# Optimization experiments

Hardware: AMD Instinct MI355X
Metric: run time of the kernel (lower is better)

## Reference

```python
import jax, jax.numpy as jnp
import numpy as np

N = 50000          # nodes
E = 600000         # edges
D = 128            # g_dim = h1_dim = h2_dim
R = 8              # 2 * n_speakers**2, n_speakers=2
B = 10             # num_bases


def setup_inputs() -> dict:
    key = jax.random.key(0)
    ks = jax.random.split(key, 10)
    s = 1.0 / np.sqrt(D)
    return {
        "node_features": jax.random.normal(ks[0], (N, D), jnp.float32),
        "edge_index": jax.random.randint(ks[1], (2, E), 0, N, jnp.int64),
        "edge_type": jax.random.randint(ks[2], (E,), 0, R, jnp.int64),
        # RGCNConv params (basis decomposition)
        "basis": jax.random.normal(ks[3], (B, D, D), jnp.float32) * s,
        "comp": jax.random.normal(ks[4], (R, B), jnp.float32) * (1.0 / np.sqrt(B)),
        "root": jax.random.normal(ks[5], (D, D), jnp.float32) * s,
        "bias1": jnp.zeros((D,), jnp.float32),
        # GraphConv params
        "w_rel": jax.random.normal(ks[6], (D, D), jnp.float32) * s,
        "b_rel": jnp.zeros((D,), jnp.float32),
        "w_root": jax.random.normal(ks[7], (D, D), jnp.float32) * s,
    }


def reference(node_features, edge_index, edge_type, basis, comp, root, bias1, w_rel, b_rel, w_root):
    x = node_features
    n = x.shape[0]
    r = comp.shape[0]
    src, dst = edge_index[0], edge_index[1]

    # ---- RGCNConv (basis decomposition, per-relation mean aggregation) ----
    # project through bases once: [N, B, D]
    xb = jnp.einsum('ni,bio->nbo', x, basis)
    # per-edge message: combine bases with relation coefficients  [E, D]
    msg = jnp.einsum('eb,ebo->eo', comp[edge_type], xb[src])
    # per-(dst, relation) mean normalization
    seg = dst * r + edge_type                       # [E]
    cnt = jax.ops.segment_sum(jnp.ones((msg.shape[0],), x.dtype), seg, num_segments=n * r)
    norm = 1.0 / jnp.maximum(cnt[seg], 1.0)         # [E]
    agg = jax.ops.segment_sum(msg * norm[:, None], dst, num_segments=n)  # [N, D]
    h1 = agg + x @ root + bias1

    # ---- GraphConv (add aggregation of neighbors + root transform) ----
    nbr = jax.ops.segment_sum(h1[src], dst, num_segments=n)  # [N, D]
    out = nbr @ w_rel.T + b_rel + h1 @ w_root.T
    return out
```

## Files before the change

### kernel.cpp

```cpp
#include <hip/hip_runtime.h>
#include <stdint.h>

#define N_NODES 50000
#define E_EDGES 600000
#define D 128
#define R_REL 8
#define B_BASES 10
#define RN (R_REL * N_NODES)

typedef __attribute__((ext_vector_type(8))) short bf16x8;
typedef __attribute__((ext_vector_type(4))) float f32x4;

__device__ __forceinline__ short f2b(float f) {
    uint32_t u = __float_as_uint(f);
    u += 0x7fff + ((u >> 16) & 1);
    return (short)(u >> 16);
}
__device__ __forceinline__ float b2f(uint16_t u) {
    return __uint_as_float((uint32_t)u << 16);
}

__global__ __launch_bounds__(256) void k_front(const float* __restrict__ x,
                                               unsigned short* __restrict__ xb,
                                               const int* __restrict__ dst,
                                               const int* __restrict__ et,
                                               int* __restrict__ cntr,
                                               const float* __restrict__ basis,
                                               const float* __restrict__ comp,
                                               const float* __restrict__ root,
                                               const float* __restrict__ wrel,
                                               const float* __restrict__ wroot,
                                               short* __restrict__ wt,
                                               short* __restrict__ wrel_b,
                                               short* __restrict__ wroot_b) {
    const int XB_N = N_NODES * D / 8;
    int tid = blockIdx.x * 256 + threadIdx.x;
    if (tid < XB_N) {
        const float4* s = (const float4*)x + (size_t)tid * 2;
        float4 v0 = s[0], v1 = s[1];
        union { uint4 u; unsigned short h[8]; } pk;
        pk.h[0] = (unsigned short)f2b(v0.x); pk.h[1] = (unsigned short)f2b(v0.y);
        pk.h[2] = (unsigned short)f2b(v0.z); pk.h[3] = (unsigned short)f2b(v0.w);
        pk.h[4] = (unsigned short)f2b(v1.x); pk.h[5] = (unsigned short)f2b(v1.y);
        pk.h[6] = (unsigned short)f2b(v1.z); pk.h[7] = (unsigned short)f2b(v1.w);
        ((uint4*)xb)[tid] = pk.u;
    } else if (tid < XB_N + E_EDGES) {
        int e = tid - XB_N;
        atomicAdd(&cntr[dst[e] * R_REL + et[e]], 1);
    } else {
        int t2 = tid - XB_N - E_EDGES;
        if (t2 < 9 * D * D) {
            int s = t2 >> 14;
            int rem = t2 & 16383;
            int j = rem >> 7, i = rem & 127;
            float v;
            if (s < 8) {
                v = 0.f;
#pragma unroll
                for (int b = 0; b < B_BASES; b++)
                    v += comp[s * B_BASES + b] * basis[b * D * D + i * D + j];
            } else {
                v = root[i * D + j];
            }
            wt[t2] = f2b(v);
        } else {
            int t3 = t2 - 9 * D * D;
            if (t3 < D * D) {
                wrel_b[t3]  = f2b(wrel[t3]);
                wroot_b[t3] = f2b(wroot[t3]);
            }
        }
    }
}

__device__ __forceinline__ int wave_scan_incl(int v) {
    int lane = threadIdx.x & 63;
#pragma unroll
    for (int off = 1; off < 64; off <<= 1) {
        int n = __shfl_up(v, off, 64);
        if (lane >= off) v += n;
    }
    return v;
}

__global__ __launch_bounds__(1024) void k_scan_a(const int* __restrict__ in,
                                                 int* __restrict__ out,
                                                 int* __restrict__ bsum, int n) {
    __shared__ int wsum[16];
    int t = threadIdx.x, lane = t & 63, wid = t >> 6;
    int g = blockIdx.x * 1024 + t;
    int v = (g < n) ? in[g] : 0;
    int isc = wave_scan_incl(v);
    if (lane == 63) wsum[wid] = isc;
    __syncthreads();
    if (wid == 0) {
        int wv = (lane < 16) ? wsum[lane] : 0;
        int wsc = wave_scan_incl(wv);
        if (lane < 16) wsum[lane] = wsc - wv;
    }
    __syncthreads();
    if (g < n) out[g] = wsum[wid] + isc - v;
    if (t == 1023 && bsum) bsum[blockIdx.x] = wsum[15] + isc;
}

__global__ __launch_bounds__(1024) void k_scan_c(int* __restrict__ out,
                                                 const int* __restrict__ bsum, int n) {
    int g = blockIdx.x * 1024 + threadIdx.x;
    if (g < n) out[g] += bsum[blockIdx.x];
}

__global__ __launch_bounds__(256) void k_bucket(const int* __restrict__ src,
                                                const int* __restrict__ dst,
                                                const int* __restrict__ et,
                                                int* __restrict__ seg_off,
                                                int* __restrict__ es1) {
    int e = blockIdx.x * 256 + threadIdx.x;
    if (e >= E_EDGES) return;
    int key = dst[e] * R_REL + et[e];
    int pos = atomicAdd(&seg_off[key], 1);
    es1[pos] = src[e];
}

__global__ __launch_bounds__(256) void k_aggmean(const unsigned short* __restrict__ xb,
                                                 const int* __restrict__ es1,
                                                 const int* __restrict__ seg_off,
                                                 unsigned short* __restrict__ mx) {
    int t = threadIdx.x;
    int sw = t >> 4, l = t & 15;
    int k = blockIdx.x * 16 + sw;
    if (k >= RN) return;
    int start = (k == 0) ? 0 : seg_off[k - 1];
    int end = seg_off[k];
    float ax[8];
#pragma unroll
    for (int q = 0; q < 8; q++) ax[q] = 0.f;
    size_t loff = (size_t)l * 8;
    int pos = start;
    for (; pos + 2 <= end; pos += 2) {
        int s0 = es1[pos], s1 = es1[pos + 1];
        uint4 v0 = *(const uint4*)(xb + (size_t)s0 * D + loff);
        uint4 v1 = *(const uint4*)(xb + (size_t)s1 * D + loff);
        const uint32_t* w0 = (const uint32_t*)&v0;
        const uint32_t* w1 = (const uint32_t*)&v1;
#pragma unroll
        for (int q = 0; q < 4; q++) {
            ax[q * 2]     += b2f((uint16_t)w0[q]) + b2f((uint16_t)w1[q]);
            ax[q * 2 + 1] += b2f((uint16_t)(w0[q] >> 16)) + b2f((uint16_t)(w1[q] >> 16));
        }
    }
    if (pos < end) {
        int s0 = es1[pos];
        uint4 v0 = *(const uint4*)(xb + (size_t)s0 * D + loff);
        const uint32_t* w0 = (const uint32_t*)&v0;
#pragma unroll
        for (int q = 0; q < 4; q++) {
            ax[q * 2]     += b2f((uint16_t)w0[q]);
            ax[q * 2 + 1] += b2f((uint16_t)(w0[q] >> 16));
        }
    }
    float nm = (end > start) ? 1.f / (float)(end - start) : 0.f;
    union { uint4 u; unsigned short h[8]; } pk;
#pragma unroll
    for (int q = 0; q < 8; q++) pk.h[q] = (unsigned short)f2b(ax[q] * nm);
    *(uint4*)(mx + (size_t)k * D + loff) = pk.u;
}

__global__ __launch_bounds__(256) void k_h1_gemm(const unsigned short* __restrict__ mx,
                                                 const unsigned short* __restrict__ xb,
                                                 const short* __restrict__ wt,
                                                 const float* __restrict__ bias1,
                                                 unsigned short* __restrict__ h1b) {
    __shared__ short ws[2][128 * 128];
    int t = threadIdx.x;
    int wave = t >> 6, lane = t & 63, quad = lane >> 4, l16 = lane & 15;
    int base = blockIdx.x * 128;
    int n0 = base + wave * 32 + l16;
    int n1 = n0 + 16;
    int nc0 = n0 < N_NODES ? n0 : N_NODES - 1;
    int nc1 = n1 < N_NODES ? n1 : N_NODES - 1;
    int ci0 = wave * 8;

    auto aptr = [&](int nc, int s) -> const unsigned short* {
        return (s < 8) ? mx + ((size_t)nc * 8 + s) * D : xb + (size_t)nc * D;
    };

    uint4 aReg[2][2][4];
    {
        uint4 b0[8];
#pragma unroll
        for (int i = 0; i < 8; i++) {
            int row = (ci0 + i) * 4 + quad;
            b0[i] = *(const uint4*)(wt + row * D + (l16 << 3));
        }
#pragma unroll
        for (int kc = 0; kc < 4; kc++) {
            int co = (kc * 4 + quad) * 8;
            aReg[0][0][kc] = *(const uint4*)(aptr(nc0, 0) + co);
            aReg[0][1][kc] = *(const uint4*)(aptr(nc1, 0) + co);
            aReg[1][0][kc] = *(const uint4*)(aptr(nc0, 1) + co);
            aReg[1][1][kc] = *(const uint4*)(aptr(nc1, 1) + co);
        }
#pragma unroll
        for (int i = 0; i < 8; i++) {
            int row = (ci0 + i) * 4 + quad;
            *(uint4*)&ws[0][row * 128 + ((l16 ^ (row & 15)) << 3)] = b0[i];
        }
    }
    __syncthreads();

    f32x4 acc[2][8];
#pragma unroll
    for (int tl = 0; tl < 2; tl++)
#pragma unroll
        for (int jt = 0; jt < 8; jt++) acc[tl][jt] = (f32x4){0.f, 0.f, 0.f, 0.f};

    for (int s = 0; s < 9; s++) {
        int cur = s & 1;
        uint4 bn[8];
        if (s + 1 < 9) {
            const short* wb = wt + (size_t)(s + 1) * D * D;
#pragma unroll
            for (int i = 0; i < 8; i++) {
                int row = (ci0 + i) * 4 + quad;
                bn[i] = *(const uint4*)(wb + row * D + (l16 << 3));
            }
        }
#pragma unroll
        for (int kc = 0; kc < 4; kc++) {
            int c0 = kc * 4 + quad;
            bf16x8 a0 = *(bf16x8*)&aReg[cur][0][kc];
            bf16x8 a1 = *(bf16x8*)&aReg[cur][1][kc];
#pragma unroll
            for (int jt = 0; jt < 8; jt++) {
                bf16x8 b = *(const bf16x8*)&ws[cur][(jt * 16 + l16) * 128 + ((c0 ^ l16) << 3)];
                acc[0][jt] = __builtin_amdgcn_mfma_f32_16x16x32_bf16(a0, b, acc[0][jt], 0, 0, 0);
                acc[1][jt] = __builtin_amdgcn_mfma_f32_16x16x32_bf16(a1, b, acc[1][jt], 0, 0, 0);
            }
        }
        if (s + 2 <= 8) {
#pragma unroll
            for (int kc = 0; kc < 4; kc++) {
                int co = (kc * 4 + quad) * 8;
                aReg[cur][0][kc] = *(const uint4*)(aptr(nc0, s + 2) + co);
                aReg[cur][1][kc] = *(const uint4*)(aptr(nc1, s + 2) + co);
            }
        }
        if (s + 1 < 9) {
#pragma unroll
            for (int i = 0; i < 8; i++) {
                int row = (ci0 + i) * 4 + quad;
                *(uint4*)&ws[cur ^ 1][row * 128 + ((l16 ^ (row & 15)) << 3)] = bn[i];
            }
        }
        __syncthreads();
    }

#pragma unroll
    for (int tl = 0; tl < 2; tl++) {
#pragma unroll
        for (int reg = 0; reg < 4; reg++) {
            int node = base + wave * 32 + tl * 16 + quad * 4 + reg;
            if (node >= N_NODES) continue;
#pragma unroll
            for (int jt = 0; jt < 8; jt++) {
                int col = jt * 16 + l16;
                float v = acc[tl][jt][reg] + bias1[col];
                h1b[(size_t)node * D + col] = (unsigned short)f2b(v);
            }
        }
    }
}

__global__ __launch_bounds__(256) void k_agg_nbr(const unsigned short* __restrict__ h1b,
                                                 const int* __restrict__ es1,
                                                 const int* __restrict__ seg_off,
                                                 unsigned short* __restrict__ nbr) {
    int t = threadIdx.x;
    int wave = t >> 6, lane = t & 63, sub = lane >> 4, l = lane & 15;
    int d = blockIdx.x * 16 + wave * 4 + sub;
    if (d >= N_NODES) return;
    int start = (d == 0) ? 0 : seg_off[d * R_REL - 1];
    int end = seg_off[d * R_REL + 7];
    float acc[8];
#pragma unroll
    for (int j = 0; j < 8; j++) acc[j] = 0.f;
    size_t loff = (size_t)l * 8;

    int pos = start;
    for (; pos + 4 <= end; pos += 4) {
        int i0 = es1[pos], i1 = es1[pos + 1], i2 = es1[pos + 2], i3 = es1[pos + 3];
        uint4 v0 = *(const uint4*)(h1b + (size_t)i0 * D + loff);
        uint4 v1 = *(const uint4*)(h1b + (size_t)i1 * D + loff);
        uint4 v2 = *(const uint4*)(h1b + (size_t)i2 * D + loff);
        uint4 v3 = *(const uint4*)(h1b + (size_t)i3 * D + loff);
        const uint32_t* w0 = (const uint32_t*)&v0;
        const uint32_t* w1 = (const uint32_t*)&v1;
        const uint32_t* w2 = (const uint32_t*)&v2;
        const uint32_t* w3 = (const uint32_t*)&v3;
#pragma unroll
        for (int q = 0; q < 4; q++) {
            acc[q * 2]     += b2f((uint16_t)w0[q]) + b2f((uint16_t)w1[q]) +
                              b2f((uint16_t)w2[q]) + b2f((uint16_t)w3[q]);
            acc[q * 2 + 1] += b2f((uint16_t)(w0[q] >> 16)) + b2f((uint16_t)(w1[q] >> 16)) +
                              b2f((uint16_t)(w2[q] >> 16)) + b2f((uint16_t)(w3[q] >> 16));
        }
    }
    for (; pos < end; pos++) {
        int i0 = es1[pos];
        uint4 v0 = *(const uint4*)(h1b + (size_t)i0 * D + loff);
        const uint32_t* w0 = (const uint32_t*)&v0;
#pragma unroll
        for (int q = 0; q < 4; q++) {
            acc[q * 2]     += b2f((uint16_t)w0[q]);
            acc[q * 2 + 1] += b2f((uint16_t)(w0[q] >> 16));
        }
    }

    union { uint4 u; unsigned short h[8]; } pk;
#pragma unroll
    for (int j = 0; j < 8; j++) pk.h[j] = (unsigned short)f2b(acc[j]);
    *(uint4*)(nbr + (size_t)d * D + loff) = pk.u;
}

__global__ __launch_bounds__(256) void k_out2(const unsigned short* __restrict__ h1b,
                                              const unsigned short* __restrict__ nbr,
                                              const short* __restrict__ wroot_b,
                                              const short* __restrict__ wrel_b,
                                              const float* __restrict__ brel,
                                              float* __restrict__ out) {
    __shared__ short ws[2][128 * 128];
    int t = threadIdx.x;
    int wave = t >> 6, lane = t & 63, quad = lane >> 4, l16 = lane & 15;
    int base = blockIdx.x * 128;
    int n0 = base + wave * 32 + l16;
    int n1 = n0 + 16;
    int nc0 = n0 < N_NODES ? n0 : N_NODES - 1;
    int nc1 = n1 < N_NODES ? n1 : N_NODES - 1;
    int ci0 = wave * 8;

    uint4 aReg[2][2][4];
    {
        uint4 b0[8];
#pragma unroll
        for (int i = 0; i < 8; i++) {
            int row = (ci0 + i) * 4 + quad;
            b0[i] = *(const uint4*)(wroot_b + row * D + (l16 << 3));
        }
#pragma unroll
        for (int kc = 0; kc < 4; kc++) {
            int co = (kc * 4 + quad) * 8;
            aReg[0][0][kc] = *(const uint4*)(h1b + (size_t)nc0 * D + co);
            aReg[0][1][kc] = *(const uint4*)(h1b + (size_t)nc1 * D + co);
            aReg[1][0][kc] = *(const uint4*)(nbr + (size_t)nc0 * D + co);
            aReg[1][1][kc] = *(const uint4*)(nbr + (size_t)nc1 * D + co);
        }
#pragma unroll
        for (int i = 0; i < 8; i++) {
            int row = (ci0 + i) * 4 + quad;
            *(uint4*)&ws[0][row * 128 + ((l16 ^ (row & 15)) << 3)] = b0[i];
        }
    }
    __syncthreads();

    f32x4 acc[2][8];
#pragma unroll
    for (int tl = 0; tl < 2; tl++)
#pragma unroll
        for (int jt = 0; jt < 8; jt++) acc[tl][jt] = (f32x4){0.f, 0.f, 0.f, 0.f};

#pragma unroll
    for (int s = 0; s < 2; s++) {
        int cur = s & 1;
        uint4 bn[8];
        if (s == 0) {
#pragma unroll
            for (int i = 0; i < 8; i++) {
                int row = (ci0 + i) * 4 + quad;
                bn[i] = *(const uint4*)(wrel_b + row * D + (l16 << 3));
            }
        }
#pragma unroll
        for (int kc = 0; kc < 4; kc++) {
            int c0 = kc * 4 + quad;
            bf16x8 a0 = *(bf16x8*)&aReg[cur][0][kc];
            bf16x8 a1 = *(bf16x8*)&aReg[cur][1][kc];
#pragma unroll
            for (int jt = 0; jt < 8; jt++) {
                bf16x8 b = *(const bf16x8*)&ws[cur][(jt * 16 + l16) * 128 + ((c0 ^ l16) << 3)];
                acc[0][jt] = __builtin_amdgcn_mfma_f32_16x16x32_bf16(a0, b, acc[0][jt], 0, 0, 0);
                acc[1][jt] = __builtin_amdgcn_mfma_f32_16x16x32_bf16(a1, b, acc[1][jt], 0, 0, 0);
            }
        }
        if (s == 0) {
#pragma unroll
            for (int i = 0; i < 8; i++) {
                int row = (ci0 + i) * 4 + quad;
                *(uint4*)&ws[1][row * 128 + ((l16 ^ (row & 15)) << 3)] = bn[i];
            }
            __syncthreads();
        }
    }

#pragma unroll
    for (int tl = 0; tl < 2; tl++) {
#pragma unroll
        for (int reg = 0; reg < 4; reg++) {
            int node = base + wave * 32 + tl * 16 + quad * 4 + reg;
            if (node >= N_NODES) continue;
#pragma unroll
            for (int jt = 0; jt < 8; jt++) {
                int col = jt * 16 + l16;
                out[(size_t)node * D + col] = acc[tl][jt][reg] + brel[col];
            }
        }
    }
}

extern "C" void kernel_launch(void* const* d_in, const int* in_sizes, int n_in,
                              void* d_out, int out_size, void* d_ws, size_t ws_size,
                              hipStream_t stream) {
    const float* x     = (const float*)d_in[0];
    const int*   ei    = (const int*)d_in[1];
    const int*   et    = (const int*)d_in[2];
    const float* basis = (const float*)d_in[3];
    const float* comp  = (const float*)d_in[4];
    const float* root  = (const float*)d_in[5];
    const float* bias1 = (const float*)d_in[6];
    const float* wrel  = (const float*)d_in[7];
    const float* brel  = (const float*)d_in[8];
    const float* wroot = (const float*)d_in[9];
    float* out = (float*)d_out;
    const int* src = ei;
    const int* dst = ei + E_EDGES;

    char* p = (char*)d_ws;
    auto alloc = [&](size_t bytes) { char* q = p; p += (bytes + 255) & ~(size_t)255; return q; };
    short* wt      = (short*)alloc((size_t)9 * D * D * sizeof(short));
    short* wrel_b  = (short*)alloc(D * D * sizeof(short));
    short* wroot_b = (short*)alloc(D * D * sizeof(short));
    int*   cntr    = (int*)alloc((size_t)RN * sizeof(int));
    int*   seg_off = (int*)alloc((size_t)RN * sizeof(int));
    int*   es1     = (int*)alloc((size_t)(E_EDGES + 16) * sizeof(int));
    int*   bsum    = (int*)alloc(1024 * sizeof(int));
    unsigned short* xb  = (unsigned short*)alloc((size_t)N_NODES * D * sizeof(unsigned short));
    unsigned short* mx  = (unsigned short*)alloc((size_t)RN * D * sizeof(unsigned short));
    unsigned short* h1b = (unsigned short*)alloc((size_t)N_NODES * D * sizeof(unsigned short));
    unsigned short* nbr = xb;

    hipMemsetAsync(cntr, 0, (size_t)RN * sizeof(int), stream);

    const int XB_N = N_NODES * D / 8;
    int nfront = (XB_N + E_EDGES + 9 * D * D + D * D + 255) / 256;
    k_front<<<nfront, 256, 0, stream>>>(x, xb, dst, et, cntr,
                                        basis, comp, root, wrel, wroot,
                                        wt, wrel_b, wroot_b);

    int nscan = (RN + 1023) / 1024;
    k_scan_a<<<nscan, 1024, 0, stream>>>(cntr, seg_off, bsum, RN);
    k_scan_a<<<1, 1024, 0, stream>>>(bsum, bsum, nullptr, nscan);
    k_scan_c<<<nscan, 1024, 0, stream>>>(seg_off, bsum, RN);

    k_bucket<<<(E_EDGES + 255) / 256, 256, 0, stream>>>(src, dst, et, seg_off, es1);

    k_aggmean<<<RN / 16, 256, 0, stream>>>(xb, es1, seg_off, mx);

    int nb2 = (N_NODES + 127) / 128;
    int na = (N_NODES + 15) / 16;
    k_h1_gemm<<<nb2, 256, 0, stream>>>(mx, xb, wt, bias1, h1b);
    k_agg_nbr<<<na, 256, 0, stream>>>(h1b, es1, seg_off, nbr);
    k_out2<<<nb2, 256, 0, stream>>>(h1b, nbr, wroot_b, wrel_b, brel, out);
}
```

Baseline: 264.7 us.

## Reorder GraphConv as transform-then-aggregate and fuse into h1 GEMM kernel

Uses linearity to compute g1 = h1·Wroot and g2 = h1·Wrel inside the h1 GEMM kernel, staging h1 through shared memory, so neighbour aggregation gathers g2 and the final kernel adds g1 and the bias directly. This drops the separate nbr buffer, the h1b round trip and the third GEMM launch, merging three kernels into two. The A-operand loads in the h1 GEMM also become nontemporal. The gather still reads bf16 rows of the same size, so gather traffic is unchanged. The trade-offs are extra shared-memory passes and syncs in the GEMM kernel and a different bf16 rounding point.

```diff
diff --git a/kernel.cpp b/kernel.cpp
--- a/kernel.cpp
+++ b/kernel.cpp
@@ -10,6 +10,7 @@
 
 typedef __attribute__((ext_vector_type(8))) short bf16x8;
 typedef __attribute__((ext_vector_type(4))) float f32x4;
+typedef __attribute__((ext_vector_type(4))) unsigned int u32x4;
 
 __device__ __forceinline__ short f2b(float f) {
     uint32_t u = __float_as_uint(f);
@@ -165,11 +166,14 @@
     *(uint4*)(mx + (size_t)k * D + loff) = pk.u;
 }
 
-__global__ __launch_bounds__(256) void k_h1_gemm(const unsigned short* __restrict__ mx,
-                                                 const unsigned short* __restrict__ xb,
-                                                 const short* __restrict__ wt,
-                                                 const float* __restrict__ bias1,
-                                                 unsigned short* __restrict__ h1b) {
+__global__ __launch_bounds__(256) void k_h1g(const unsigned short* __restrict__ mx,
+                                             const unsigned short* __restrict__ xb,
+                                             const short* __restrict__ wt,
+                                             const float* __restrict__ bias1,
+                                             const short* __restrict__ wroot_b,
+                                             const short* __restrict__ wrel_b,
+                                             unsigned short* __restrict__ g1,
+                                             unsigned short* __restrict__ g2) {
     __shared__ short ws[2][128 * 128];
     int t = threadIdx.x;
     int wave = t >> 6, lane = t & 63, quad = lane >> 4, l16 = lane & 15;
@@ -184,7 +188,7 @@
         return (s < 8) ? mx + ((size_t)nc * 8 + s) * D : xb + (size_t)nc * D;
     };
 
-    uint4 aReg[2][2][4];
+    u32x4 aReg[2][2][4];
     {
         uint4 b0[8];
 #pragma unroll
@@ -195,10 +199,10 @@
 #pragma unroll
         for (int kc = 0; kc < 4; kc++) {
             int co = (kc * 4 + quad) * 8;
-            aReg[0][0][kc] = *(const uint4*)(aptr(nc0, 0) + co);
-            aReg[0][1][kc] = *(const uint4*)(aptr(nc1, 0) + co);
-            aReg[1][0][kc] = *(const uint4*)(aptr(nc0, 1) + co);
-            aReg[1][1][kc] = *(const uint4*)(aptr(nc1, 1) + co);
+            aReg[0][0][kc] = __builtin_nontemporal_load((const u32x4*)(aptr(nc0, 0) + co));
+            aReg[0][1][kc] = __builtin_nontemporal_load((const u32x4*)(aptr(nc1, 0) + co));
+            aReg[1][0][kc] = __builtin_nontemporal_load((const u32x4*)(aptr(nc0, 1) + co));
+            aReg[1][1][kc] = __builtin_nontemporal_load((const u32x4*)(aptr(nc1, 1) + co));
         }
 #pragma unroll
         for (int i = 0; i < 8; i++) {
@@ -241,8 +245,8 @@
 #pragma unroll
             for (int kc = 0; kc < 4; kc++) {
                 int co = (kc * 4 + quad) * 8;
-                aReg[cur][0][kc] = *(const uint4*)(aptr(nc0, s + 2) + co);
-                aReg[cur][1][kc] = *(const uint4*)(aptr(nc1, s + 2) + co);
+                aReg[cur][0][kc] = __builtin_nontemporal_load((const u32x4*)(aptr(nc0, s + 2) + co));
+                aReg[cur][1][kc] = __builtin_nontemporal_load((const u32x4*)(aptr(nc1, s + 2) + co));
             }
         }
         if (s + 1 < 9) {
@@ -255,6 +259,53 @@
         __syncthreads();
     }
 
+    uint4 bw[8];
+#pragma unroll
+    for (int i = 0; i < 8; i++) {
+        int row = (ci0 + i) * 4 + quad;
+        bw[i] = *(const uint4*)(wroot_b + row * D + (l16 << 3));
+    }
+#pragma unroll
+    for (int tl = 0; tl < 2; tl++) {
+#pragma unroll
+        for (int reg = 0; reg < 4; reg++) {
+            int row = wave * 32 + tl * 16 + quad * 4 + reg;
+            int swz = row & 15;
+#pragma unroll
+            for (int jt = 0; jt < 8; jt++) {
+                int col = jt * 16 + l16;
+                float v = acc[tl][jt][reg] + bias1[col];
+                ws[0][row * 128 + (((col >> 3) ^ swz) << 3) + (col & 7)] = f2b(v);
+            }
+        }
+    }
+#pragma unroll
+    for (int i = 0; i < 8; i++) {
+        int row = (ci0 + i) * 4 + quad;
+        *(uint4*)&ws[1][row * 128 + ((l16 ^ (row & 15)) << 3)] = bw[i];
+    }
+    __syncthreads();
+#pragma unroll
+    for (int i = 0; i < 8; i++) {
+        int row = (ci0 + i) * 4 + quad;
+        bw[i] = *(const uint4*)(wrel_b + row * D + (l16 << 3));
+    }
+#pragma unroll
+    for (int tl = 0; tl < 2; tl++)
+#pragma unroll
+        for (int jt = 0; jt < 8; jt++) acc[tl][jt] = (f32x4){0.f, 0.f, 0.f, 0.f};
+#pragma unroll
+    for (int kc = 0; kc < 4; kc++) {
+        int c0 = kc * 4 + quad;
+        bf16x8 a0 = *(const bf16x8*)&ws[0][(wave * 32 + l16) * 128 + ((c0 ^ l16) << 3)];
+        bf16x8 a1 = *(const bf16x8*)&ws[0][(wave * 32 + 16 + l16) * 128 + ((c0 ^ l16) << 3)];
+#pragma unroll
+        for (int jt = 0; jt < 8; jt++) {
+            bf16x8 b = *(const bf16x8*)&ws[1][(jt * 16 + l16) * 128 + ((c0 ^ l16) << 3)];
+            acc[0][jt] = __builtin_amdgcn_mfma_f32_16x16x32_bf16(a0, b, acc[0][jt], 0, 0, 0);
+            acc[1][jt] = __builtin_amdgcn_mfma_f32_16x16x32_bf16(a1, b, acc[1][jt], 0, 0, 0);
+        }
+    }
 #pragma unroll
     for (int tl = 0; tl < 2; tl++) {
 #pragma unroll
@@ -262,19 +313,52 @@
             int node = base + wave * 32 + tl * 16 + quad * 4 + reg;
             if (node >= N_NODES) continue;
 #pragma unroll
-            for (int jt = 0; jt < 8; jt++) {
-                int col = jt * 16 + l16;
-                float v = acc[tl][jt][reg] + bias1[col];
-                h1b[(size_t)node * D + col] = (unsigned short)f2b(v);
-            }
-        }
-    }
-}
-
-__global__ __launch_bounds__(256) void k_agg_nbr(const unsigned short* __restrict__ h1b,
-                                                 const int* __restrict__ es1,
-                                                 const int* __restrict__ seg_off,
-                                                 unsigned short* __restrict__ nbr) {
+            for (int jt = 0; jt < 8; jt++)
+                g1[(size_t)node * D + jt * 16 + l16] = (unsigned short)f2b(acc[tl][jt][reg]);
+        }
+    }
+    __syncthreads();
+#pragma unroll
+    for (int i = 0; i < 8; i++) {
+        int row = (ci0 + i) * 4 + quad;
+        *(uint4*)&ws[1][row * 128 + ((l16 ^ (row & 15)) << 3)] = bw[i];
+    }
+    __syncthreads();
+#pragma unroll
+    for (int tl = 0; tl < 2; tl++)
+#pragma unroll
+        for (int jt = 0; jt < 8; jt++) acc[tl][jt] = (f32x4){0.f, 0.f, 0.f, 0.f};
+#pragma unroll
+    for (int kc = 0; kc < 4; kc++) {
+        int c0 = kc * 4 + quad;
+        bf16x8 a0 = *(const bf16x8*)&ws[0][(wave * 32 + l16) * 128 + ((c0 ^ l16) << 3)];
+        bf16x8 a1 = *(const bf16x8*)&ws[0][(wave * 32 + 16 + l16) * 128 + ((c0 ^ l16) << 3)];
+#pragma unroll
+        for (int jt = 0; jt < 8; jt++) {
+            bf16x8 b = *(const bf16x8*)&ws[1][(jt * 16 + l16) * 128 + ((c0 ^ l16) << 3)];
+            acc[0][jt] = __builtin_amdgcn_mfma_f32_16x16x32_bf16(a0, b, acc[0][jt], 0, 0, 0);
+            acc[1][jt] = __builtin_amdgcn_mfma_f32_16x16x32_bf16(a1, b, acc[1][jt], 0, 0, 0);
+        }
+    }
+#pragma unroll
+    for (int tl = 0; tl < 2; tl++) {
+#pragma unroll
+        for (int reg = 0; reg < 4; reg++) {
+            int node = base + wave * 32 + tl * 16 + quad * 4 + reg;
+            if (node >= N_NODES) continue;
+#pragma unroll
+            for (int jt = 0; jt < 8; jt++)
+                g2[(size_t)node * D + jt * 16 + l16] = (unsigned short)f2b(acc[tl][jt][reg]);
+        }
+    }
+}
+
+__global__ __launch_bounds__(256) void k_final(const unsigned short* __restrict__ g1,
+                                               const unsigned short* __restrict__ g2,
+                                               const int* __restrict__ es1,
+                                               const int* __restrict__ seg_off,
+                                               const float* __restrict__ brel,
+                                               float* __restrict__ out) {
     int t = threadIdx.x;
     int wave = t >> 6, lane = t & 63, sub = lane >> 4, l = lane & 15;
     int d = blockIdx.x * 16 + wave * 4 + sub;
@@ -289,10 +373,10 @@
     int pos = start;
     for (; pos + 4 <= end; pos += 4) {
         int i0 = es1[pos], i1 = es1[pos + 1], i2 = es1[pos + 2], i3 = es1[pos + 3];
-        uint4 v0 = *(const uint4*)(h1b + (size_t)i0 * D + loff);
-        uint4 v1 = *(const uint4*)(h1b + (size_t)i1 * D + loff);
-        uint4 v2 = *(const uint4*)(h1b + (size_t)i2 * D + loff);
-        uint4 v3 = *(const uint4*)(h1b + (size_t)i3 * D + loff);
+        uint4 v0 = *(const uint4*)(g2 + (size_t)i0 * D + loff);
+        uint4 v1 = *(const uint4*)(g2 + (size_t)i1 * D + loff);
+        uint4 v2 = *(const uint4*)(g2 + (size_t)i2 * D + loff);
+        uint4 v3 = *(const uint4*)(g2 + (size_t)i3 * D + loff);
         const uint32_t* w0 = (const uint32_t*)&v0;
         const uint32_t* w1 = (const uint32_t*)&v1;
         const uint32_t* w2 = (const uint32_t*)&v2;
@@ -307,7 +391,7 @@
     }
     for (; pos < end; pos++) {
         int i0 = es1[pos];
-        uint4 v0 = *(const uint4*)(h1b + (size_t)i0 * D + loff);
+        uint4 v0 = *(const uint4*)(g2 + (size_t)i0 * D + loff);
         const uint32_t* w0 = (const uint32_t*)&v0;
 #pragma unroll
         for (int q = 0; q < 4; q++) {
@@ -316,104 +400,20 @@
         }
     }
 
-    union { uint4 u; unsigned short h[8]; } pk;
-#pragma unroll
-    for (int j = 0; j < 8; j++) pk.h[j] = (unsigned short)f2b(acc[j]);
-    *(uint4*)(nbr + (size_t)d * D + loff) = pk.u;
-}
-
-__global__ __launch_bounds__(256) void k_out2(const unsigned short* __restrict__ h1b,
-                                              const unsigned short* __restrict__ nbr,
-                                              const short* __restrict__ wroot_b,
-                                              const short* __restrict__ wrel_b,
-                                              const float* __restrict__ brel,
-                                              float* __restrict__ out) {
-    __shared__ short ws[2][128 * 128];
-    int t = threadIdx.x;
-    int wave = t >> 6, lane = t & 63, quad = lane >> 4, l16 = lane & 15;
-    int base = blockIdx.x * 128;
-    int n0 = base + wave * 32 + l16;
-    int n1 = n0 + 16;
-    int nc0 = n0 < N_NODES ? n0 : N_NODES - 1;
-    int nc1 = n1 < N_NODES ? n1 : N_NODES - 1;
-    int ci0 = wave * 8;
-
-    uint4 aReg[2][2][4];
-    {
-        uint4 b0[8];
-#pragma unroll
-        for (int i = 0; i < 8; i++) {
-            int row = (ci0 + i) * 4 + quad;
-            b0[i] = *(const uint4*)(wroot_b + row * D + (l16 << 3));
-        }
-#pragma unroll
-        for (int kc = 0; kc < 4; kc++) {
-            int co = (kc * 4 + quad) * 8;
-            aReg[0][0][kc] = *(const uint4*)(h1b + (size_t)nc0 * D + co);
-            aReg[0][1][kc] = *(const uint4*)(h1b + (size_t)nc1 * D + co);
-            aReg[1][0][kc] = *(const uint4*)(nbr + (size_t)nc0 * D + co);
-            aReg[1][1][kc] = *(const uint4*)(nbr + (size_t)nc1 * D + co);
-        }
-#pragma unroll
-        for (int i = 0; i < 8; i++) {
-            int row = (ci0 + i) * 4 + quad;
-            *(uint4*)&ws[0][row * 128 + ((l16 ^ (row & 15)) << 3)] = b0[i];
-        }
-    }
-    __syncthreads();
-
-    f32x4 acc[2][8];
-#pragma unroll
-    for (int tl = 0; tl < 2; tl++)
-#pragma unroll
-        for (int jt = 0; jt < 8; jt++) acc[tl][jt] = (f32x4){0.f, 0.f, 0.f, 0.f};
-
-#pragma unroll
-    for (int s = 0; s < 2; s++) {
-        int cur = s & 1;
-        uint4 bn[8];
-        if (s == 0) {
-#pragma unroll
-            for (int i = 0; i < 8; i++) {
-                int row = (ci0 + i) * 4 + quad;
-                bn[i] = *(const uint4*)(wrel_b + row * D + (l16 << 3));
-            }
-        }
-#pragma unroll
-        for (int kc = 0; kc < 4; kc++) {
-            int c0 = kc * 4 + quad;
-            bf16x8 a0 = *(bf16x8*)&aReg[cur][0][kc];
-            bf16x8 a1 = *(bf16x8*)&aReg[cur][1][kc];
-#pragma unroll
-            for (int jt = 0; jt < 8; jt++) {
-                bf16x8 b = *(const bf16x8*)&ws[cur][(jt * 16 + l16) * 128 + ((c0 ^ l16) << 3)];
-                acc[0][jt] = __builtin_amdgcn_mfma_f32_16x16x32_bf16(a0, b, acc[0][jt], 0, 0, 0);
-                acc[1][jt] = __builtin_amdgcn_mfma_f32_16x16x32_bf16(a1, b, acc[1][jt], 0, 0, 0);
-            }
-        }
-        if (s == 0) {
-#pragma unroll
-            for (int i = 0; i < 8; i++) {
-                int row = (ci0 + i) * 4 + quad;
-                *(uint4*)&ws[1][row * 128 + ((l16 ^ (row & 15)) << 3)] = bn[i];
-            }
-            __syncthreads();
-        }
-    }
-
-#pragma unroll
-    for (int tl = 0; tl < 2; tl++) {
-#pragma unroll
-        for (int reg = 0; reg < 4; reg++) {
-            int node = base + wave * 32 + tl * 16 + quad * 4 + reg;
-            if (node >= N_NODES) continue;
-#pragma unroll
-            for (int jt = 0; jt < 8; jt++) {
-                int col = jt * 16 + l16;
-                out[(size_t)node * D + col] = acc[tl][jt][reg] + brel[col];
-            }
-        }
-    }
+    uint4 gv = *(const uint4*)(g1 + (size_t)d * D + loff);
+    const uint32_t* gw = (const uint32_t*)&gv;
+    float4 b0 = *(const float4*)(brel + l * 8);
+    float4 b1 = *(const float4*)(brel + l * 8 + 4);
+    float bv[8] = {b0.x, b0.y, b0.z, b0.w, b1.x, b1.y, b1.z, b1.w};
+    float o[8];
+#pragma unroll
+    for (int q = 0; q < 4; q++) {
+        o[q * 2]     = acc[q * 2] + b2f((uint16_t)gw[q]) + bv[q * 2];
+        o[q * 2 + 1] = acc[q * 2 + 1] + b2f((uint16_t)(gw[q] >> 16)) + bv[q * 2 + 1];
+    }
+    float* orow = out + (size_t)d * D + loff;
+    *(float4*)orow = make_float4(o[0], o[1], o[2], o[3]);
+    *(float4*)(orow + 4) = make_float4(o[4], o[5], o[6], o[7]);
 }
 
 extern "C" void kernel_launch(void* const* d_in, const int* in_sizes, int n_in,
@@ -444,8 +444,8 @@
     int*   bsum    = (int*)alloc(1024 * sizeof(int));
     unsigned short* xb  = (unsigned short*)alloc((size_t)N_NODES * D * sizeof(unsigned short));
     unsigned short* mx  = (unsigned short*)alloc((size_t)RN * D * sizeof(unsigned short));
-    unsigned short* h1b = (unsigned short*)alloc((size_t)N_NODES * D * sizeof(unsigned short));
-    unsigned short* nbr = xb;
+    unsigned short* g1  = (unsigned short*)alloc((size_t)N_NODES * D * sizeof(unsigned short));
+    unsigned short* g2  = (unsigned short*)alloc((size_t)N_NODES * D * sizeof(unsigned short));
 
     hipMemsetAsync(cntr, 0, (size_t)RN * sizeof(int), stream);
 
@@ -466,7 +466,6 @@
 
     int nb2 = (N_NODES + 127) / 128;
     int na = (N_NODES + 15) / 16;
-    k_h1_gemm<<<nb2, 256, 0, stream>>>(mx, xb, wt, bias1, h1b);
-    k_agg_nbr<<<na, 256, 0, stream>>>(h1b, es1, seg_off, nbr);
-    k_out2<<<nb2, 256, 0, stream>>>(h1b, nbr, wroot_b, wrel_b, brel, out);
-}
+    k_h1g<<<nb2, 256, 0, stream>>>(mx, xb, wt, bias1, wroot_b, wrel_b, g1, g2);
+    k_final<<<na, 256, 0, stream>>>(g1, g2, es1, seg_off, brel, out);
+}
```

Result: slower. 284.3 us (+7.4%).
